# Optimization experiments

Hardware: AMD Instinct MI355X
Metric: run time of the kernel (lower is better)

Reference implementation:

```python
import jax, jax.numpy as jnp
import numpy as np

NUM_EXPERTS = 8
HIDDEN = 1024
INTERMEDIATE = 4096
TOKENS_PER_EXPERT = 2048


def _init_uniform(key, shape):
    # mirrors init_: uniform(-std, std) with std = 1/sqrt(last_dim)
    std = 1.0 / np.sqrt(shape[-1])
    return jax.random.uniform(key, shape, dtype=jnp.float32, minval=-std, maxval=std)


def setup_inputs() -> dict:
    key = jax.random.key(0)
    kx, k1, k2 = jax.random.split(key, 3)
    x = jax.random.normal(kx, (NUM_EXPERTS, TOKENS_PER_EXPERT, HIDDEN), dtype=jnp.float32)
    w1 = _init_uniform(k1, (NUM_EXPERTS, HIDDEN, INTERMEDIATE))
    w2 = _init_uniform(k2, (NUM_EXPERTS, INTERMEDIATE, HIDDEN))
    return {"x": x, "w1": w1, "w2": w2}


def reference(x, w1, w2):
    # grouped GEMM over experts: [e,n,d] @ [e,d,h] -> [e,n,h]
    hidden = jnp.einsum('end,edh->enh', x, w1)
    hidden = jax.nn.gelu(hidden, approximate=False)  # torch nn.GELU default = exact erf
    out = jnp.einsum('enh,ehd->end', hidden, w2)
    return out
```

## Files before the change

kernel.cpp:

```cpp
#include <hip/hip_runtime.h>
#include <hip/hip_bf16.h>
#include <math.h>

#define NE 8
#define MM 2048
#define DH 1024
#define DI 4096

#define BK  32
#define LDA 40

typedef short bf16x8 __attribute__((ext_vector_type(8)));
typedef float f32x4  __attribute__((ext_vector_type(4)));

__device__ __forceinline__ unsigned short f2bf(float f) {
    unsigned u = __builtin_bit_cast(unsigned, f);
    u += 0x7FFFu + ((u >> 16) & 1u);
    return (unsigned short)(u >> 16);
}

__device__ __forceinline__ void gload_lds16(const void* g, void* l) {
    __builtin_amdgcn_global_load_lds(
        (__attribute__((address_space(1))) void*)g,
        (__attribute__((address_space(3))) void*)l, 16, 0, 0);
}

__device__ __forceinline__ float gelu_fast(float x) {
    float z = fabsf(x) * 0.70710678118654752f;
    float t = __builtin_amdgcn_rcpf(1.0f + 0.3275911f * z);
    float p = t * (0.254829592f + t * (-0.284496736f + t * (1.421413741f +
              t * (-1.453152027f + t * 1.061405429f))));
    float er = 1.0f - p * __expf(-z * z);
    er = (x < 0.0f) ? -er : er;
    return 0.5f * x * (1.0f + er);
}

__global__ __launch_bounds__(256)
void convert_bf16(const float* __restrict__ in, unsigned short* __restrict__ out,
                  long long n)
{
    long long i = ((long long)blockIdx.x * 256 + threadIdx.x) * 8;
    const float4 v0 = *(const float4*)(in + i);
    const float4 v1 = *(const float4*)(in + i + 4);
    bf16x8 s;
    s[0] = (short)f2bf(v0.x); s[1] = (short)f2bf(v0.y);
    s[2] = (short)f2bf(v0.z); s[3] = (short)f2bf(v0.w);
    s[4] = (short)f2bf(v1.x); s[5] = (short)f2bf(v1.y);
    s[6] = (short)f2bf(v1.z); s[7] = (short)f2bf(v1.w);
    *(bf16x8*)(out + i) = s;
}

__global__ __launch_bounds__(256)
void transpose_bf16(const float* __restrict__ in, unsigned short* __restrict__ out,
                    int K, int N)
{
    __shared__ short tile[64][66];
    const int e  = blockIdx.z;
    const int n0 = blockIdx.x * 64;
    const int k0 = blockIdx.y * 64;
    const float* ine = in + (size_t)e * K * N;
    unsigned short* oute = out + (size_t)e * N * K;
    const int tid = threadIdx.x;

    #pragma unroll
    for (int i = 0; i < 4; ++i) {
        int idx = tid + i * 256;
        int r  = idx >> 4;
        int c  = (idx & 15) * 4;
        const float4 v = *(const float4*)(ine + (size_t)(k0 + r) * N + n0 + c);
        tile[r][c + 0] = (short)f2bf(v.x);
        tile[r][c + 1] = (short)f2bf(v.y);
        tile[r][c + 2] = (short)f2bf(v.z);
        tile[r][c + 3] = (short)f2bf(v.w);
    }
    __syncthreads();
    #pragma unroll
    for (int i = 0; i < 4; ++i) {
        int idx = tid + i * 256;
        int n  = idx >> 4;
        int k  = (idx & 15) * 4;
        short4 s;
        s.x = tile[k + 0][n];
        s.y = tile[k + 1][n];
        s.z = tile[k + 2][n];
        s.w = tile[k + 3][n];
        *(short4*)(oute + (size_t)(n0 + n) * K + k0 + k) = s;
    }
}


#define VMC(n)  asm volatile("s_waitcnt vmcnt(" #n ")" ::: "memory")
#define LGKM0   do { asm volatile("s_waitcnt lgkmcnt(0)" ::: "memory"); \
                     __builtin_amdgcn_sched_barrier(0); } while (0)
#define BARX    do { __builtin_amdgcn_s_barrier(); \
                     __builtin_amdgcn_sched_barrier(0); } while (0)
#define PRIO1   __builtin_amdgcn_s_setprio(1)
#define PRIO0   __builtin_amdgcn_s_setprio(0)

#define STAGE(Ptr, r0, s, t, KD, DstArr)                                       \
    { const size_t kk = (size_t)(t) * 64;                                      \
      _Pragma("unroll")                                                        \
      for (int j = 0; j < 4; ++j) {                                            \
          int idx = tid + j * 512;                                             \
          int row = idx >> 3;                                                  \
          int gs  = (idx & 7) ^ (row & 7);                                     \
          gload_lds16(Ptr + (size_t)((r0) + row) * (KD) + kk + gs * 8,         \
                      &DstArr[s][(j * 512 + wave * 64) * 8]); } }

#define LOAD_A(s, h)                                                           \
    _Pragma("unroll")                                                          \
    for (int mi = 0; mi < 4; ++mi) {                                           \
        int r = wm2 * 128 + (h) * 64 + mi * 16 + lr;                           \
        _Pragma("unroll")                                                      \
        for (int ks = 0; ks < 2; ++ks)                                         \
            a[mi][ks] = *(const bf16x8*)(&As[s][r * 64 +                       \
                          (((ks * 4 + lq) ^ (lr & 7)) * 8)]);                  \
    }

#define LOAD_B(s)                                                              \
    _Pragma("unroll")                                                          \
    for (int ni = 0; ni < 4; ++ni) {                                           \
        int r = wn4 * 64 + ni * 16 + lr;                                       \
        _Pragma("unroll")                                                      \
        for (int ks = 0; ks < 2; ++ks)                                         \
            b[ni][ks] = *(const bf16x8*)(&Bs[s][r * 64 +                       \
                          (((ks * 4 + lq) ^ (lr & 7)) * 8)]);                  \
    }

#define MFMA_HALF(h)                                                           \
    _Pragma("unroll")                                                          \
    for (int mi = 0; mi < 4; ++mi)                                             \
        _Pragma("unroll")                                                      \
        for (int ni = 0; ni < 4; ++ni)                                         \
            _Pragma("unroll")                                                  \
            for (int ks = 0; ks < 2; ++ks)                                     \
                acc[(h) * 4 + mi][ni] = __builtin_amdgcn_mfma_f32_16x16x32_bf16( \
                    a[mi][ks], b[ni][ks], acc[(h) * 4 + mi][ni], 0, 0, 0);

#define PIPE_BODY(KD)                                                          \
    __shared__ short As[2][256 * 64];                                          \
    __shared__ short Bs[2][256 * 64];                                          \
    const int tid  = threadIdx.x;                                              \
    const int lane = tid & 63;                                                 \
    const int wave = tid >> 6;                                                 \
    const int wm2  = wave >> 2;                                                \
    const int wn4  = wave & 3;                                                 \
    const int lr   = lane & 15;                                                \
    const int lq   = lane >> 4;                                                \
    const int NI   = (KD) / 128;                                               \
    f32x4 acc[8][4] = {};                                                      \
    bf16x8 a[4][2], b[4][2];                                                   \
    STAGE(Ae, m0, 0, 0, KD, As); STAGE(Be, n0, 0, 0, KD, Bs);                  \
    STAGE(Be, n0, 1, 1, KD, Bs);                                               \
    VMC(4); BARX;                                                              \
    _Pragma("unroll 1")                                                        \
    for (int i = 0; i < NI; ++i) {                                             \
        const bool nl = (i < NI - 1);                                          \
                                                  \
        STAGE(Ae, m0, 1, 2 * i + 1, KD, As);                                   \
        LOAD_B(0); LOAD_A(0, 0);                                               \
        LGKM0; PRIO1; MFMA_HALF(0); PRIO0; BARX;                               \
                                                  \
        if (nl) STAGE(Be, n0, 0, 2 * i + 2, KD, Bs);                           \
        LOAD_A(0, 1);                                                          \
        LGKM0; PRIO1; MFMA_HALF(1); PRIO0;                                     \
        if (nl) { VMC(4); } else { VMC(0); }                                   \
        BARX;                                                                  \
                                                  \
        if (nl) STAGE(Ae, m0, 0, 2 * i + 2, KD, As);                           \
        LOAD_B(1); LOAD_A(1, 0);                                               \
        LGKM0; PRIO1; MFMA_HALF(0); PRIO0; BARX;                               \
                                                  \
        if (nl) STAGE(Be, n0, 1, 2 * i + 3, KD, Bs);                           \
        LOAD_A(1, 1);                                                          \
        LGKM0; PRIO1; MFMA_HALF(1); PRIO0;                                     \
        if (nl) VMC(4);                                                        \
        BARX;                                                                  \
    }

#define DECOMPOSE_XCD_V3(TPE)                                                  \
    const int bsw  = (blockIdx.x & 7) * (TPE) + (blockIdx.x >> 3);             \
    const int e    = bsw / (TPE);                                              \
    const int trem = bsw - e * (TPE);                                          \
    const int m0   = (trem & 7) * 256;                                         \
    const int n0   = (trem >> 3) * 256;

__global__ __launch_bounds__(512, 2)
void gemm1_v3(const unsigned short* __restrict__ Xb,
              const unsigned short* __restrict__ W1t,
              unsigned short* __restrict__ H)
{
    DECOMPOSE_XCD_V3(128)
    const unsigned short* Ae = Xb  + (size_t)e * MM * DH;
    const unsigned short* Be = W1t + (size_t)e * DI * DH;
    unsigned short* He = H + (size_t)e * MM * DI;

    PIPE_BODY(DH)

    #pragma unroll
    for (int mi = 0; mi < 8; ++mi) {
        #pragma unroll
        for (int ni = 0; ni < 4; ++ni) {
            const int col = n0 + wn4 * 64 + ni * 16 + lr;
            #pragma unroll
            for (int r = 0; r < 4; ++r) {
                const int row = m0 + wm2 * 128 + mi * 16 + lq * 4 + r;
                He[(size_t)row * DI + col] = f2bf(gelu_fast(acc[mi][ni][r]));
            }
        }
    }
}

__global__ __launch_bounds__(512, 2)
void gemm2_v3(const unsigned short* __restrict__ H,
              const unsigned short* __restrict__ W2t,
              float* __restrict__ O)
{
    DECOMPOSE_XCD_V3(32)
    const unsigned short* Ae = H   + (size_t)e * MM * DI;
    const unsigned short* Be = W2t + (size_t)e * DH * DI;
    float* Oe = O + (size_t)e * MM * DH;

    PIPE_BODY(DI)

    #pragma unroll
    for (int mi = 0; mi < 8; ++mi) {
        #pragma unroll
        for (int ni = 0; ni < 4; ++ni) {
            const int col = n0 + wn4 * 64 + ni * 16 + lr;
            #pragma unroll
            for (int r = 0; r < 4; ++r) {
                const int row = m0 + wm2 * 128 + mi * 16 + lq * 4 + r;
                Oe[(size_t)row * DH + col] = acc[mi][ni][r];
            }
        }
    }
}

__global__ __launch_bounds__(256, 2)
void gemm1_mixed(const float* __restrict__ X, const unsigned short* __restrict__ W1t,
                 unsigned short* __restrict__ H)
{
    __shared__ short As[128 * LDA];
    __shared__ short Bs[128 * 32];
    const int e  = blockIdx.z;
    const int m0 = blockIdx.y * 128;
    const int n0 = blockIdx.x * 128;
    const float* Xe = X + (size_t)e * MM * DH;
    const unsigned short* Bt = W1t + (size_t)e * DI * DH;
    unsigned short* He = H + (size_t)e * MM * DI;
    const int tid  = threadIdx.x;
    const int lane = tid & 63;
    const int wave = tid >> 6;
    const int wm = (wave >> 1) * 64;
    const int wn = (wave &  1) * 64;
    const int lr = lane & 15;
    const int lq = lane >> 4;
    f32x4 acc[4][4] = {};
    for (int k0 = 0; k0 < DH; k0 += BK) {
        #pragma unroll
        for (int i = 0; i < 2; ++i) {
            int idx  = tid + i * 256;
            gload_lds16(Bt + (size_t)(n0 + (idx >> 2)) * DH + k0 + (idx & 3) * 8,
                        Bs + (i * 256 + wave * 64) * 8);
        }
        #pragma unroll
        for (int i = 0; i < 4; ++i) {
            int idx = tid + i * 256;
            int row = idx >> 3;
            int col = (idx & 7) * 4;
            const float4 v = *(const float4*)(Xe + (size_t)(m0 + row) * DH + k0 + col);
            short4 s;
            s.x = (short)f2bf(v.x); s.y = (short)f2bf(v.y);
            s.z = (short)f2bf(v.z); s.w = (short)f2bf(v.w);
            *(short4*)(&As[row * LDA + col]) = s;
        }
        __syncthreads();
        bf16x8 a[4], b[4];
        #pragma unroll
        for (int i = 0; i < 4; ++i)
            a[i] = *(const bf16x8*)(&As[(wm + i * 16 + lr) * LDA + lq * 8]);
        #pragma unroll
        for (int i = 0; i < 4; ++i)
            b[i] = *(const bf16x8*)(&Bs[(wn + i * 16 + lr) * 32 + lq * 8]);
        #pragma unroll
        for (int mi = 0; mi < 4; ++mi)
            #pragma unroll
            for (int ni = 0; ni < 4; ++ni)
                acc[mi][ni] = __builtin_amdgcn_mfma_f32_16x16x32_bf16(a[mi], b[ni], acc[mi][ni], 0, 0, 0);
        __syncthreads();
    }
    #pragma unroll
    for (int mi = 0; mi < 4; ++mi) {
        #pragma unroll
        for (int ni = 0; ni < 4; ++ni) {
            const int col = n0 + wn + ni * 16 + lr;
            #pragma unroll
            for (int r = 0; r < 4; ++r) {
                const int row = m0 + wm + mi * 16 + lq * 4 + r;
                He[(size_t)row * DI + col] = f2bf(gelu_fast(acc[mi][ni][r]));
            }
        }
    }
}

__global__ __launch_bounds__(256, 2)
void fb_gemm1(const float* __restrict__ X, const float* __restrict__ W1,
              unsigned short* __restrict__ H)
{
    __shared__ short As[128 * LDA];
    __shared__ short Bs[128 * LDA];
    const int e  = blockIdx.z;
    const int m0 = blockIdx.y * 128;
    const int n0 = blockIdx.x * 128;
    const float* Xe  = X  + (size_t)e * MM * DH;
    const float* W1e = W1 + (size_t)e * DH * DI;
    unsigned short* He = H + (size_t)e * MM * DI;
    const int tid  = threadIdx.x;
    const int lane = tid & 63;
    const int wave = tid >> 6;
    const int wm = (wave >> 1) * 64;
    const int wn = (wave &  1) * 64;
    const int lr = lane & 15;
    const int lq = lane >> 4;
    f32x4 acc[4][4] = {};
    for (int k0 = 0; k0 < DH; k0 += BK) {
        #pragma unroll
        for (int i = 0; i < 4; ++i) {
            int idx = tid + i * 256;
            int row = idx >> 3;
            int col = (idx & 7) * 4;
            const float4 v = *(const float4*)(Xe + (size_t)(m0 + row) * DH + k0 + col);
            short4 s;
            s.x = (short)f2bf(v.x); s.y = (short)f2bf(v.y);
            s.z = (short)f2bf(v.z); s.w = (short)f2bf(v.w);
            *(short4*)(&As[row * LDA + col]) = s;
        }
        #pragma unroll
        for (int i = 0; i < 4; ++i) {
            int idx  = tid + i * 256;
            int krow = idx >> 5;
            int ncol = (idx & 31) * 4;
            const float4 v = *(const float4*)(W1e + (size_t)(k0 + krow) * DI + n0 + ncol);
            Bs[(ncol + 0) * LDA + krow] = (short)f2bf(v.x);
            Bs[(ncol + 1) * LDA + krow] = (short)f2bf(v.y);
            Bs[(ncol + 2) * LDA + krow] = (short)f2bf(v.z);
            Bs[(ncol + 3) * LDA + krow] = (short)f2bf(v.w);
        }
        __syncthreads();
        bf16x8 a[4], b[4];
        #pragma unroll
        for (int i = 0; i < 4; ++i)
            a[i] = *(const bf16x8*)(&As[(wm + i * 16 + lr) * LDA + lq * 8]);
        #pragma unroll
        for (int i = 0; i < 4; ++i)
            b[i] = *(const bf16x8*)(&Bs[(wn + i * 16 + lr) * LDA + lq * 8]);
        #pragma unroll
        for (int mi = 0; mi < 4; ++mi)
            #pragma unroll
            for (int ni = 0; ni < 4; ++ni)
                acc[mi][ni] = __builtin_amdgcn_mfma_f32_16x16x32_bf16(a[mi], b[ni], acc[mi][ni], 0, 0, 0);
        __syncthreads();
    }
    #pragma unroll
    for (int mi = 0; mi < 4; ++mi) {
        #pragma unroll
        for (int ni = 0; ni < 4; ++ni) {
            const int col = n0 + wn + ni * 16 + lr;
            #pragma unroll
            for (int r = 0; r < 4; ++r) {
                const int row = m0 + wm + mi * 16 + lq * 4 + r;
                He[(size_t)row * DI + col] = f2bf(gelu_fast(acc[mi][ni][r]));
            }
        }
    }
}

__global__ __launch_bounds__(256, 2)
void fb_gemm2(const unsigned short* __restrict__ H, const float* __restrict__ W2,
              float* __restrict__ O)
{
    __shared__ short As[128 * LDA];
    __shared__ short Bs[128 * LDA];
    const int e  = blockIdx.z;
    const int m0 = blockIdx.y * 128;
    const int n0 = blockIdx.x * 128;
    const unsigned short* He = H + (size_t)e * MM * DI;
    const float* W2e = W2 + (size_t)e * DI * DH;
    float* Oe = O + (size_t)e * MM * DH;
    const int tid  = threadIdx.x;
    const int lane = tid & 63;
    const int wave = tid >> 6;
    const int wm = (wave >> 1) * 64;
    const int wn = (wave &  1) * 64;
    const int lr = lane & 15;
    const int lq = lane >> 4;
    f32x4 acc[4][4] = {};
    for (int k0 = 0; k0 < DI; k0 += BK) {
        #pragma unroll
        for (int i = 0; i < 2; ++i) {
            int idx = tid + i * 256;
            int row = idx >> 2;
            int col = (idx & 3) * 8;
            bf16x8 v = *(const bf16x8*)(He + (size_t)(m0 + row) * DI + k0 + col);
            *(bf16x8*)(&As[row * LDA + col]) = v;
        }
        #pragma unroll
        for (int i = 0; i < 4; ++i) {
            int idx  = tid + i * 256;
            int krow = idx >> 5;
            int ncol = (idx & 31) * 4;
            const float4 v = *(const float4*)(W2e + (size_t)(k0 + krow) * DH + n0 + ncol);
            Bs[(ncol + 0) * LDA + krow] = (short)f2bf(v.x);
            Bs[(ncol + 1) * LDA + krow] = (short)f2bf(v.y);
            Bs[(ncol + 2) * LDA + krow] = (short)f2bf(v.z);
            Bs[(ncol + 3) * LDA + krow] = (short)f2bf(v.w);
        }
        __syncthreads();
        bf16x8 a[4], b[4];
        #pragma unroll
        for (int i = 0; i < 4; ++i)
            a[i] = *(const bf16x8*)(&As[(wm + i * 16 + lr) * LDA + lq * 8]);
        #pragma unroll
        for (int i = 0; i < 4; ++i)
            b[i] = *(const bf16x8*)(&Bs[(wn + i * 16 + lr) * LDA + lq * 8]);
        #pragma unroll
        for (int mi = 0; mi < 4; ++mi)
            #pragma unroll
            for (int ni = 0; ni < 4; ++ni)
                acc[mi][ni] = __builtin_amdgcn_mfma_f32_16x16x32_bf16(a[mi], b[ni], acc[mi][ni], 0, 0, 0);
        __syncthreads();
    }
    #pragma unroll
    for (int mi = 0; mi < 4; ++mi) {
        #pragma unroll
        for (int ni = 0; ni < 4; ++ni) {
            const int col = n0 + wn + ni * 16 + lr;
            #pragma unroll
            for (int r = 0; r < 4; ++r) {
                const int row = m0 + wm + mi * 16 + lq * 4 + r;
                Oe[(size_t)row * DH + col] = acc[mi][ni][r];
            }
        }
    }
}

extern "C" void kernel_launch(void* const* d_in, const int* in_sizes, int n_in,
                              void* d_out, int out_size, void* d_ws, size_t ws_size,
                              hipStream_t stream) {
    const float* x  = (const float*)d_in[0];
    const float* w1 = (const float*)d_in[1];
    const float* w2 = (const float*)d_in[2];
    float* out = (float*)d_out;

    const size_t WT_BYTES     = (size_t)NE * DH * DI * 2;
    const size_t HIDDEN_BYTES = (size_t)NE * MM * DI * 2;
    const size_t XB_BYTES     = (size_t)NE * MM * DH * 2;

    dim3 blk(256), blk512(512);
    if (ws_size >= WT_BYTES + HIDDEN_BYTES + XB_BYTES) {
        unsigned short* wt     = (unsigned short*)d_ws;
        unsigned short* hidden = (unsigned short*)((char*)d_ws + WT_BYTES);
        unsigned short* xb     = (unsigned short*)((char*)d_ws + WT_BYTES + HIDDEN_BYTES);
        const long long nx = (long long)NE * MM * DH;
        convert_bf16<<<dim3((unsigned)(nx / (8 * 256))), blk, 0, stream>>>(x, xb, nx);
        transpose_bf16<<<dim3(DI / 64, DH / 64, NE), blk, 0, stream>>>(w1, wt, DH, DI);
        gemm1_v3<<<dim3(NE * (MM / 256) * (DI / 256)), blk512, 0, stream>>>(xb, wt, hidden);
        transpose_bf16<<<dim3(DH / 64, DI / 64, NE), blk, 0, stream>>>(w2, wt, DI, DH);
        gemm2_v3<<<dim3(NE * (MM / 256) * (DH / 256)), blk512, 0, stream>>>(hidden, wt, out);
    } else if (ws_size >= WT_BYTES + HIDDEN_BYTES) {
        unsigned short* wt     = (unsigned short*)d_ws;
        unsigned short* hidden = (unsigned short*)((char*)d_ws + WT_BYTES);
        transpose_bf16<<<dim3(DI / 64, DH / 64, NE), blk, 0, stream>>>(w1, wt, DH, DI);
        gemm1_mixed<<<dim3(DI / 128, MM / 128, NE), blk, 0, stream>>>(x, wt, hidden);
        transpose_bf16<<<dim3(DH / 64, DI / 64, NE), blk, 0, stream>>>(w2, wt, DI, DH);
        gemm2_v3<<<dim3(NE * (MM / 256) * (DH / 256)), blk512, 0, stream>>>(hidden, wt, out);
    } else {
        unsigned short* hidden = (unsigned short*)d_ws;
        fb_gemm1<<<dim3(DI / 128, MM / 128, NE), blk, 0, stream>>>(x, w1, hidden);
        fb_gemm2<<<dim3(DH / 128, MM / 128, NE), blk, 0, stream>>>(hidden, w2, out);
    }
}
```

Before: 640.3 us.

## Split GEMM main loop into eight half-tile stages with finer load interleaving

Rewrites the double-buffered bf16 GEMM pipeline so each 64-wide K tile is processed in eight sub-phases (per k-slice and M-half) instead of four. Global-to-LDS staging is split into half-tile chunks spread across these phases, and fragment registers shrink from [4][2] to [4]. The aim is to smooth global load issue, overlap it better with MFMA work, and reduce register pressure. The cost is twice as many barriers per iteration and more complex buffer-hazard ordering.

```diff
diff --git a/kernel.cpp b/kernel.cpp
--- a/kernel.cpp
+++ b/kernel.cpp
@@ -97,47 +97,37 @@
 #define PRIO1   __builtin_amdgcn_s_setprio(1)
 #define PRIO0   __builtin_amdgcn_s_setprio(0)
 
-#define STAGE(Ptr, r0, s, t, KD, DstArr)                                       \
+#define STAGE_H(Ptr, r0, s, t, KD, Dst, half)                                  \
     { const size_t kk = (size_t)(t) * 64;                                      \
       _Pragma("unroll")                                                        \
-      for (int j = 0; j < 4; ++j) {                                            \
+      for (int j = 0; j < 2; ++j) {                                            \
           int idx = tid + j * 512;                                             \
-          int row = idx >> 3;                                                  \
+          int row = (half) * 128 + (idx >> 3);                                 \
           int gs  = (idx & 7) ^ (row & 7);                                     \
           gload_lds16(Ptr + (size_t)((r0) + row) * (KD) + kk + gs * 8,         \
-                      &DstArr[s][(j * 512 + wave * 64) * 8]); } }
-
-#define LOAD_A(s, h)                                                           \
+                      &Dst[s][((half) * 1024 + j * 512 + wave * 64) * 8]); } }
+
+#define LOAD_B_KS(s, ks)                                                       \
     _Pragma("unroll")                                                          \
-    for (int mi = 0; mi < 4; ++mi) {                                           \
-        int r = wm2 * 128 + (h) * 64 + mi * 16 + lr;                           \
-        _Pragma("unroll")                                                      \
-        for (int ks = 0; ks < 2; ++ks)                                         \
-            a[mi][ks] = *(const bf16x8*)(&As[s][r * 64 +                       \
-                          (((ks * 4 + lq) ^ (lr & 7)) * 8)]);                  \
-    }
-
-#define LOAD_B(s)                                                              \
+    for (int ni = 0; ni < 4; ++ni)                                             \
+        b[ni] = *(const bf16x8*)(&Bs[s][(wn4 * 64 + ni * 16 + lr) * 64 +       \
+                      ((((ks) * 4 + lq) ^ (lr & 7)) * 8)]);
+
+#define LOAD_A_HK(s, mh, ks)                                                   \
     _Pragma("unroll")                                                          \
-    for (int ni = 0; ni < 4; ++ni) {                                           \
-        int r = wn4 * 64 + ni * 16 + lr;                                       \
-        _Pragma("unroll")                                                      \
-        for (int ks = 0; ks < 2; ++ks)                                         \
-            b[ni][ks] = *(const bf16x8*)(&Bs[s][r * 64 +                       \
-                          (((ks * 4 + lq) ^ (lr & 7)) * 8)]);                  \
-    }
-
-#define MFMA_HALF(h)                                                           \
+    for (int mi = 0; mi < 4; ++mi)                                             \
+        a[mi] = *(const bf16x8*)(&As[s][(wm2 * 128 + (mh) * 64 + mi * 16 + lr) * 64 + \
+                      ((((ks) * 4 + lq) ^ (lr & 7)) * 8)]);
+
+#define MFMA16(mh)                                                             \
     _Pragma("unroll")                                                          \
     for (int mi = 0; mi < 4; ++mi)                                             \
         _Pragma("unroll")                                                      \
         for (int ni = 0; ni < 4; ++ni)                                         \
-            _Pragma("unroll")                                                  \
-            for (int ks = 0; ks < 2; ++ks)                                     \
-                acc[(h) * 4 + mi][ni] = __builtin_amdgcn_mfma_f32_16x16x32_bf16( \
-                    a[mi][ks], b[ni][ks], acc[(h) * 4 + mi][ni], 0, 0, 0);
-
-#define PIPE_BODY(KD)                                                          \
+            acc[(mh) * 4 + mi][ni] = __builtin_amdgcn_mfma_f32_16x16x32_bf16(  \
+                a[mi], b[ni], acc[(mh) * 4 + mi][ni], 0, 0, 0);
+
+#define PIPE_BODY_V4(KD)                                                       \
     __shared__ short As[2][256 * 64];                                          \
     __shared__ short Bs[2][256 * 64];                                          \
     const int tid  = threadIdx.x;                                              \
@@ -147,34 +137,51 @@
     const int wn4  = wave & 3;                                                 \
     const int lr   = lane & 15;                                                \
     const int lq   = lane >> 4;                                                \
-    const int NI   = (KD) / 128;                                               \
+    const int ITERS = (KD) / 128;                                              \
     f32x4 acc[8][4] = {};                                                      \
-    bf16x8 a[4][2], b[4][2];                                                   \
-    STAGE(Ae, m0, 0, 0, KD, As); STAGE(Be, n0, 0, 0, KD, Bs);                  \
-    STAGE(Be, n0, 1, 1, KD, Bs);                                               \
-    VMC(4); BARX;                                                              \
+    bf16x8 a[4], b[4];                                                         \
+    STAGE_H(Ae, m0, 0, 0, KD, As, 0); STAGE_H(Ae, m0, 0, 0, KD, As, 1);        \
+    STAGE_H(Be, n0, 0, 0, KD, Bs, 0); STAGE_H(Be, n0, 0, 0, KD, Bs, 1);        \
+    STAGE_H(Be, n0, 1, 1, KD, Bs, 0);                                          \
+    VMC(2); BARX;                                                              \
     _Pragma("unroll 1")                                                        \
-    for (int i = 0; i < NI; ++i) {                                             \
-        const bool nl = (i < NI - 1);                                          \
-                                                  \
-        STAGE(Ae, m0, 1, 2 * i + 1, KD, As);                                   \
-        LOAD_B(0); LOAD_A(0, 0);                                               \
-        LGKM0; PRIO1; MFMA_HALF(0); PRIO0; BARX;                               \
-                                                  \
-        if (nl) STAGE(Be, n0, 0, 2 * i + 2, KD, Bs);                           \
-        LOAD_A(0, 1);                                                          \
-        LGKM0; PRIO1; MFMA_HALF(1); PRIO0;                                     \
-        if (nl) { VMC(4); } else { VMC(0); }                                   \
+    for (int i = 0; i < ITERS; ++i) {                                          \
+        const bool nl = (i < ITERS - 1);                                       \
+                                                      \
+        LOAD_B_KS(0, 0); LOAD_A_HK(0, 0, 0);                                   \
+        STAGE_H(Be, n0, 1, 2 * i + 1, KD, Bs, 1);                              \
+        BARX; LGKM0; PRIO1; MFMA16(0); PRIO0; BARX;                            \
+                                                      \
+        LOAD_A_HK(0, 1, 0);                                                    \
+        STAGE_H(Ae, m0, 1, 2 * i + 1, KD, As, 0);                              \
+        BARX; LGKM0; PRIO1; MFMA16(1); PRIO0; BARX;                            \
+                                                      \
+        LOAD_B_KS(0, 1); LOAD_A_HK(0, 0, 1);                                   \
+        STAGE_H(Ae, m0, 1, 2 * i + 1, KD, As, 1);                              \
+        BARX; LGKM0; PRIO1; MFMA16(0); PRIO0; BARX;                            \
+                                                      \
+        LOAD_A_HK(0, 1, 1);                                                    \
+        if (nl) STAGE_H(Be, n0, 0, 2 * i + 2, KD, Bs, 0);                      \
+        BARX; LGKM0; PRIO1; MFMA16(1); PRIO0;                                  \
+        if (nl) { VMC(2); } else { VMC(0); }                                   \
         BARX;                                                                  \
-                                                  \
-        if (nl) STAGE(Ae, m0, 0, 2 * i + 2, KD, As);                           \
-        LOAD_B(1); LOAD_A(1, 0);                                               \
-        LGKM0; PRIO1; MFMA_HALF(0); PRIO0; BARX;                               \
-                                                  \
-        if (nl) STAGE(Be, n0, 1, 2 * i + 3, KD, Bs);                           \
-        LOAD_A(1, 1);                                                          \
-        LGKM0; PRIO1; MFMA_HALF(1); PRIO0;                                     \
-        if (nl) VMC(4);                                                        \
+                                                      \
+        LOAD_B_KS(1, 0); LOAD_A_HK(1, 0, 0);                                   \
+        if (nl) STAGE_H(Be, n0, 0, 2 * i + 2, KD, Bs, 1);                      \
+        BARX; LGKM0; PRIO1; MFMA16(0); PRIO0; BARX;                            \
+                                                      \
+        LOAD_A_HK(1, 1, 0);                                                    \
+        if (nl) STAGE_H(Ae, m0, 0, 2 * i + 2, KD, As, 0);                      \
+        BARX; LGKM0; PRIO1; MFMA16(1); PRIO0; BARX;                            \
+                                                      \
+        LOAD_B_KS(1, 1); LOAD_A_HK(1, 0, 1);                                   \
+        if (nl) STAGE_H(Ae, m0, 0, 2 * i + 2, KD, As, 1);                      \
+        BARX; LGKM0; PRIO1; MFMA16(0); PRIO0; BARX;                            \
+                                                      \
+        LOAD_A_HK(1, 1, 1);                                                    \
+        if (nl) STAGE_H(Be, n0, 1, 2 * i + 3, KD, Bs, 0);                      \
+        BARX; LGKM0; PRIO1; MFMA16(1); PRIO0;                                  \
+        if (nl) VMC(2);                                                        \
         BARX;                                                                  \
     }
 
@@ -186,7 +193,7 @@
     const int n0   = (trem >> 3) * 256;
 
 __global__ __launch_bounds__(512, 2)
-void gemm1_v3(const unsigned short* __restrict__ Xb,
+void gemm1_v4(const unsigned short* __restrict__ Xb,
               const unsigned short* __restrict__ W1t,
               unsigned short* __restrict__ H)
 {
@@ -195,7 +202,7 @@
     const unsigned short* Be = W1t + (size_t)e * DI * DH;
     unsigned short* He = H + (size_t)e * MM * DI;
 
-    PIPE_BODY(DH)
+    PIPE_BODY_V4(DH)
 
     #pragma unroll
     for (int mi = 0; mi < 8; ++mi) {
@@ -212,7 +219,7 @@
 }
 
 __global__ __launch_bounds__(512, 2)
-void gemm2_v3(const unsigned short* __restrict__ H,
+void gemm2_v4(const unsigned short* __restrict__ H,
               const unsigned short* __restrict__ W2t,
               float* __restrict__ O)
 {
@@ -221,7 +228,7 @@
     const unsigned short* Be = W2t + (size_t)e * DH * DI;
     float* Oe = O + (size_t)e * MM * DH;
 
-    PIPE_BODY(DI)
+    PIPE_BODY_V4(DI)
 
     #pragma unroll
     for (int mi = 0; mi < 8; ++mi) {
@@ -465,16 +472,16 @@
         const long long nx = (long long)NE * MM * DH;
         convert_bf16<<<dim3((unsigned)(nx / (8 * 256))), blk, 0, stream>>>(x, xb, nx);
         transpose_bf16<<<dim3(DI / 64, DH / 64, NE), blk, 0, stream>>>(w1, wt, DH, DI);
-        gemm1_v3<<<dim3(NE * (MM / 256) * (DI / 256)), blk512, 0, stream>>>(xb, wt, hidden);
+        gemm1_v4<<<dim3(NE * (MM / 256) * (DI / 256)), blk512, 0, stream>>>(xb, wt, hidden);
         transpose_bf16<<<dim3(DH / 64, DI / 64, NE), blk, 0, stream>>>(w2, wt, DI, DH);
-        gemm2_v3<<<dim3(NE * (MM / 256) * (DH / 256)), blk512, 0, stream>>>(hidden, wt, out);
+        gemm2_v4<<<dim3(NE * (MM / 256) * (DH / 256)), blk512, 0, stream>>>(hidden, wt, out);
     } else if (ws_size >= WT_BYTES + HIDDEN_BYTES) {
         unsigned short* wt     = (unsigned short*)d_ws;
         unsigned short* hidden = (unsigned short*)((char*)d_ws + WT_BYTES);
         transpose_bf16<<<dim3(DI / 64, DH / 64, NE), blk, 0, stream>>>(w1, wt, DH, DI);
         gemm1_mixed<<<dim3(DI / 128, MM / 128, NE), blk, 0, stream>>>(x, wt, hidden);
         transpose_bf16<<<dim3(DH / 64, DI / 64, NE), blk, 0, stream>>>(w2, wt, DI, DH);
-        gemm2_v3<<<dim3(NE * (MM / 256) * (DH / 256)), blk512, 0, stream>>>(hidden, wt, out);
+        gemm2_v4<<<dim3(NE * (MM / 256) * (DH / 256)), blk512, 0, stream>>>(hidden, wt, out);
     } else {
         unsigned short* hidden = (unsigned short*)d_ws;
         fb_gemm1<<<dim3(DI / 128, MM / 128, NE), blk, 0, stream>>>(x, w1, hidden);
```

Measured after the change: 662.8 us. 1.04x slower.
